# Kernel tuning notes

Hardware: AMD Instinct MI355X
Metric: run time of the kernel (lower is better)

## Reference

```python
import jax, jax.numpy as jnp
import numpy as np

EMBED = 512
HEADS = 64
DK = EMBED // HEADS  # == n_wires_attn == 8
NW_FFN = 8
FFN = 2048
EPS = 1e-5


def _layernorm(x, g, b):
    mu = jnp.mean(x, axis=-1, keepdims=True)
    var = jnp.var(x, axis=-1, keepdims=True)
    return (x - mu) * jax.lax.rsqrt(var + EPS) * g + b


def setup_inputs() -> dict:
    key = jax.random.key(0)
    ks = jax.random.split(key, 12)
    d = {
        "x": jax.random.normal(ks[0], (4, 1024, EMBED), dtype=jnp.float32),
        # attention quantum RX params (one per wire, shared across heads/tokens)
        "phi": jax.random.normal(ks[1], (DK,), dtype=jnp.float32) * 0.1,
        # combine_heads linear
        "Wc": jax.random.normal(ks[2], (EMBED, EMBED), dtype=jnp.float32) / np.sqrt(EMBED),
        "bc": jnp.zeros((EMBED,), dtype=jnp.float32),
        # FFN quantum RY params
        "theta": jax.random.normal(ks[3], (NW_FFN,), dtype=jnp.float32) * 0.1,
        "W1": jax.random.normal(ks[4], (NW_FFN, FFN), dtype=jnp.float32) / np.sqrt(NW_FFN),
        "b1": jnp.zeros((FFN,), dtype=jnp.float32),
        "W2": jax.random.normal(ks[5], (FFN, EMBED), dtype=jnp.float32) / np.sqrt(FFN),
        "b2": jnp.zeros((EMBED,), dtype=jnp.float32),
        "g1": jnp.ones((EMBED,), dtype=jnp.float32),
        "be1": jnp.zeros((EMBED,), dtype=jnp.float32),
        "g2": jnp.ones((EMBED,), dtype=jnp.float32),
        "be2": jnp.zeros((EMBED,), dtype=jnp.float32),
    }
    return d


def reference(x, phi, Wc, bc, theta, W1, b1, W2, b2, g1, be1, g2, be2):
    B, S, E = x.shape
    # --- quantum attention projections ---
    # Per head-row of DK features: RX(x_i) encoder then trainable RX(phi_i),
    xh = x.reshape(B, S, HEADS, DK)
    qkv = jnp.cos(xh + phi)                     # [B,S,H,DK]
    qkv = jnp.transpose(qkv, (0, 2, 1, 3))      # [B,H,S,DK]
    scores = jnp.einsum('bhqd,bhkd->bhqk', qkv, qkv) / jnp.sqrt(jnp.float32(DK))
    attn = jax.nn.softmax(scores, axis=-1)
    out = jnp.einsum('bhqk,bhkd->bhqd', attn, qkv)
    out = jnp.transpose(out, (0, 2, 1, 3)).reshape(B, S, E)
    attn_out = out @ Wc.T if False else out @ Wc + bc  # combine_heads linear
    x1 = _layernorm(x + attn_out, g1, be1)
    # --- quantum FFN: RX(x_i) then trainable RY(theta_i) -> <Z> = cos(x_i)*cos(theta_i)
    qout = jnp.cos(x1[..., :NW_FFN]) * jnp.cos(theta)   # [B,S,NW_FFN]
    h = jax.nn.relu(qout @ W1 + b1)
    ffn_out = h @ W2 + b2
    return _layernorm(x1 + ffn_out, g2, be2)
```

## Files before the change

kernel.cpp:

```cpp
#include <hip/hip_runtime.h>
#include <hip/hip_bf16.h>
#include <math.h>

#define B 4
#define S 1024
#define E 512
#define H 64
#define DK 8
#define FFN 2048
#define BS (B*S)

#define CSCALE 0.7141879f

#if __has_builtin(__builtin_amdgcn_exp2f)
#define EXP2F(x) __builtin_amdgcn_exp2f(x)
#else
#define EXP2F(x) exp2f(x)
#endif

typedef __attribute__((ext_vector_type(8))) short short8;
typedef __attribute__((ext_vector_type(4))) float float4a;

union U8 { short8 v; unsigned u[4]; };
union F4 { float4a v; float f[4]; };

__device__ __forceinline__ unsigned short f2bf(float f) {
    unsigned u = __builtin_bit_cast(unsigned, f);
    u = (u + 0x7fffu + ((u >> 16) & 1u)) >> 16;
    return (unsigned short)u;
}
__device__ __forceinline__ float bf2f(unsigned short h) {
    return __builtin_bit_cast(float, (unsigned)h << 16);
}
__device__ __forceinline__ unsigned packbf(float a, float b) {
    return __builtin_amdgcn_perm(__builtin_bit_cast(unsigned, a),
                                 __builtin_bit_cast(unsigned, b), 0x07060302u);
}
__device__ __forceinline__ unsigned packbf_rn(float a, float b) {
    return ((unsigned)f2bf(a) << 16) | f2bf(b);
}
__device__ __forceinline__ int pidx(int k) {
    return (k & ~31) | (((k >> 2) & 3) << 3) | (((k >> 4) & 1) << 2) | (k & 3);
}

__global__ __launch_bounds__(512) void attn_conv_kernel(const float* __restrict__ x,
                                                        const float* __restrict__ phi,
                                                        const float* __restrict__ Wc,
                                                        const float* __restrict__ W2,
                                                        const float* __restrict__ W1,
                                                        const float* __restrict__ b1,
                                                        unsigned short* __restrict__ Afrag,
                                                        unsigned short* __restrict__ W2f,
                                                        unsigned short* __restrict__ Wcf,
                                                        unsigned short* __restrict__ W1f) {
    __shared__ unsigned short kv[(S + 16) * DK];
    __shared__ unsigned short vtp[9][S + 8];
    int bid = blockIdx.x;
    int tid = threadIdx.x;

    if (bid >= 1024) {
        int idx = (bid - 1024) * 512 + tid;
        if (idx < 131072) {
            int lane = idx & 63, c = idx >> 6;
            int ntile = c >> 6, kb32 = c & 63;
            int g = lane >> 4, col = lane & 15;
            int n = ntile * 16 + col, kb = kb32 * 32;
            short8 o;
            #pragma unroll
            for (int j = 0; j < 8; j++) {
                int k = kb + 16 * (j >> 2) + 4 * g + (j & 3);
                o[j] = (short)f2bf(W2[(size_t)k * 512 + n]);
            }
            *(short8*)&W2f[(size_t)idx * 8] = o;
        } else if (idx < 163840) {
            int i2 = idx - 131072;
            int lane = i2 & 63, c = i2 >> 6;
            int ntile = c >> 4, kb32 = c & 15;
            int g = lane >> 4, col = lane & 15;
            int n = ntile * 16 + col, kb = kb32 * 32;
            short8 o;
            #pragma unroll
            for (int j = 0; j < 8; j++)
                o[j] = (short)f2bf(Wc[(size_t)(kb + g * 8 + j) * 512 + n]);
            *(short8*)&Wcf[(size_t)i2 * 8] = o;
        } else {
            int i3 = idx - 163840;
            int lane = i3 & 63, c = i3 >> 6;
            int g = lane >> 4, col = lane & 15;
            int f = (c >> 1) * 32 + (c & 1) * 16 + col;
            short8 o = {0,0,0,0,0,0,0,0};
            if (g == 0) {
                #pragma unroll
                for (int j = 0; j < 8; j++) o[j] = (short)f2bf(W1[j * FFN + f]);
            } else if (g == 1) {
                o[0] = (short)f2bf(b1[f]);
            }
            *(short8*)&W1f[(size_t)i3 * 8] = o;
        }
        return;
    }

    int head = bid >> 2, qquad = bid & 3;
    int b = head >> 6, hh = head & 63;

    float ph[DK];
    #pragma unroll
    for (int d = 0; d < DK; d++) ph[d] = phi[d];

    const short8 z8 = {0,0,0,0,0,0,0,0};
    {
        int r2 = tid * 2;
        unsigned short vb[8][2];
        #pragma unroll
        for (int j = 0; j < 2; j++) {
            const float* xp = x + ((size_t)(b * S + r2 + j)) * E + hh * DK;
            float4 u = *(const float4*)xp;
            float4 v = *(const float4*)(xp + 4);
            float c[8] = {__cosf(u.x+ph[0]), __cosf(u.y+ph[1]), __cosf(u.z+ph[2]), __cosf(u.w+ph[3]),
                          __cosf(v.x+ph[4]), __cosf(v.y+ph[5]), __cosf(v.z+ph[6]), __cosf(v.w+ph[7])};
            U8 kr;
            kr.u[0] = packbf_rn(c[1] * CSCALE, c[0] * CSCALE);
            kr.u[1] = packbf_rn(c[3] * CSCALE, c[2] * CSCALE);
            kr.u[2] = packbf_rn(c[5] * CSCALE, c[4] * CSCALE);
            kr.u[3] = packbf_rn(c[7] * CSCALE, c[6] * CSCALE);
            *(short8*)&kv[(r2 + j) * DK] = kr.v;
            #pragma unroll
            for (int d = 0; d < 8; d++) vb[d][j] = f2bf(c[d]);
        }
        int pr = pidx(r2);
        #pragma unroll
        for (int d = 0; d < 8; d++)
            *(unsigned*)&vtp[d][pr] = (unsigned)vb[d][0] | ((unsigned)vb[d][1] << 16);
        *(unsigned*)&vtp[8][pr] = 0x3F803F80u;
    }
    if (tid < 16) *(short8*)&kv[(S + tid) * DK] = z8;
    __syncthreads();

    int w = tid >> 6, lane = tid & 63, col = lane & 15, g = lane >> 4;
    bool g0 = (g == 0);
    int q0 = qquad * 256 + w * 32;
    const float4a zc = {0.f,0.f,0.f,0.f};

    short8 aq[2];
    #pragma unroll
    for (int t = 0; t < 2; t++)
        aq[t] = g0 ? *(const short8*)&kv[(q0 + t*16 + col) * DK] : z8;

    float4a acc[2];
    acc[0] = zc; acc[1] = zc;

    int vrow = col < 8 ? col : 8;
    const unsigned short* vbase = &vtp[vrow][0];

    int off0 = g0 ? col * DK : S * DK;
    int off1 = g0 ? (16 + col) * DK : S * DK;
    int stepo = g0 ? 32 * DK : 0;

    for (int kb = 0; kb < S; kb += 32) {
        short8 bk0 = *(const short8*)&kv[off0];
        short8 bk1 = *(const short8*)&kv[off1];
        off0 += stepo; off1 += stepo;
        short8 vf = *(const short8*)(vbase + kb + g * 8);
        #pragma unroll
        for (int t = 0; t < 2; t++) {
            float4a s0 = __builtin_amdgcn_mfma_f32_16x16x32_bf16(bk0, aq[t], zc, 0,0,0);
            float4a s1 = __builtin_amdgcn_mfma_f32_16x16x32_bf16(bk1, aq[t], zc, 0,0,0);
            F4 S0, S1; S0.v = s0; S1.v = s1;
            float e00 = EXP2F(S0.f[0]);
            float e01 = EXP2F(S0.f[1]);
            float e02 = EXP2F(S0.f[2]);
            float e03 = EXP2F(S0.f[3]);
            float e10 = EXP2F(S1.f[0]);
            float e11 = EXP2F(S1.f[1]);
            float e12 = EXP2F(S1.f[2]);
            float e13 = EXP2F(S1.f[3]);
            U8 pf;
            pf.u[0] = packbf(e01, e00);
            pf.u[1] = packbf(e03, e02);
            pf.u[2] = packbf(e11, e10);
            pf.u[3] = packbf(e13, e12);
            acc[t] = __builtin_amdgcn_mfma_f32_16x16x32_bf16(vf, pf.v, acc[t], 0,0,0);
        }
    }
    int lp8 = ((hh & 3) * 16 + col) * 8;
    #pragma unroll
    for (int t = 0; t < 2; t++) {
        F4 a; a.v = acc[t];
        float denom = __shfl(a.f[0], 32 + col);
        float inv = __builtin_amdgcn_rcpf(denom);
        if (g < 2) {
            int chunk = (hh >> 2) * 256 + (b * 64 + qquad * 16 + w * 2 + t);
            uint2 o;
            o.x = packbf_rn(a.f[1] * inv, a.f[0] * inv);
            o.y = packbf_rn(a.f[3] * inv, a.f[2] * inv);
            *(uint2*)&Afrag[(size_t)chunk * 512 + lp8 + g * 4] = o;
        }
    }
}

__global__ __launch_bounds__(512) void combine_ln1(const unsigned short* __restrict__ Afrag,
                                                   const unsigned short* __restrict__ Wcf,
                                                   const float* __restrict__ bc,
                                                   const float* __restrict__ x,
                                                   const float* __restrict__ g1,
                                                   const float* __restrict__ be1,
                                                   float* __restrict__ x1out,
                                                   unsigned short* __restrict__ qoutbf,
                                                   const float* __restrict__ theta) {
    __shared__ unsigned short As[16 * 64 * 8];
    __shared__ float xout[16][516];
    int tt = blockIdx.x;
    int tid = threadIdx.x;

    for (int i = tid; i < 1024; i += 512)
        *(short8*)&As[i * 8] =
            *(const short8*)&Afrag[((size_t)((i >> 6) * 256 + tt) * 64 + (i & 63)) * 8];
    __syncthreads();

    int w = tid >> 6, lane = tid & 63, col = lane & 15, g = lane >> 4;
    const float4a zc = {0.f,0.f,0.f,0.f};
    float4a acc[4];
    #pragma unroll
    for (int nt = 0; nt < 4; nt++) acc[nt] = zc;

    for (int kb32 = 0; kb32 < 16; kb32++) {
        short8 af = *(const short8*)&As[(kb32 * 64 + lane) * 8];
        #pragma unroll
        for (int nt = 0; nt < 4; nt++) {
            short8 bf = *(const short8*)&Wcf[((size_t)((w * 4 + nt) * 16 + kb32) * 64 + lane) * 8];
            acc[nt] = __builtin_amdgcn_mfma_f32_16x16x32_bf16(af, bf, acc[nt], 0, 0, 0);
        }
    }
    #pragma unroll
    for (int nt = 0; nt < 4; nt++) {
        int n = w * 64 + nt * 16 + col;
        float bb = bc[n];
        #pragma unroll
        for (int r = 0; r < 4; r++)
            xout[g * 4 + r][n] = acc[nt][r] + bb;
    }
    __syncthreads();

    int hl = lane >> 5, l = lane & 31;
    int token = w * 2 + hl;
    int e0 = l * 16;
    size_t grow = ((size_t)tt * 16 + token) * 512;
    float v[16];
    float s = 0.f, sq = 0.f;
    #pragma unroll
    for (int u = 0; u < 4; u++) {
        float4 xv = *(const float4*)&x[grow + e0 + u * 4];
        float4 pv = *(const float4*)&xout[token][e0 + u * 4];
        float a0 = xv.x + pv.x, a1 = xv.y + pv.y, a2 = xv.z + pv.z, a3 = xv.w + pv.w;
        v[u*4] = a0; v[u*4+1] = a1; v[u*4+2] = a2; v[u*4+3] = a3;
        s += a0 + a1 + a2 + a3;
        sq += a0*a0 + a1*a1 + a2*a2 + a3*a3;
    }
    #pragma unroll
    for (int off = 1; off <= 16; off <<= 1) {
        s  += __shfl_xor(s, off);
        sq += __shfl_xor(sq, off);
    }
    float mu = s * (1.f / 512.f);
    float var = sq * (1.f / 512.f) - mu * mu;
    float rstd = rsqrtf(var + 1e-5f);
    float y[16];
    #pragma unroll
    for (int u = 0; u < 4; u++) {
        float4 gv = *(const float4*)&g1[e0 + u * 4];
        float4 bv = *(const float4*)&be1[e0 + u * 4];
        y[u*4]   = (v[u*4]   - mu) * rstd * gv.x + bv.x;
        y[u*4+1] = (v[u*4+1] - mu) * rstd * gv.y + bv.y;
        y[u*4+2] = (v[u*4+2] - mu) * rstd * gv.z + bv.z;
        y[u*4+3] = (v[u*4+3] - mu) * rstd * gv.w + bv.w;
        float4 o = make_float4(y[u*4], y[u*4+1], y[u*4+2], y[u*4+3]);
        *(float4*)&x1out[grow + e0 + u * 4] = o;
    }
    if (l == 0) {
        U8 q;
        q.u[0] = packbf_rn(__cosf(y[1]) * __cosf(theta[1]), __cosf(y[0]) * __cosf(theta[0]));
        q.u[1] = packbf_rn(__cosf(y[3]) * __cosf(theta[3]), __cosf(y[2]) * __cosf(theta[2]));
        q.u[2] = packbf_rn(__cosf(y[5]) * __cosf(theta[5]), __cosf(y[4]) * __cosf(theta[4]));
        q.u[3] = packbf_rn(__cosf(y[7]) * __cosf(theta[7]), __cosf(y[6]) * __cosf(theta[6]));
        *(short8*)&qoutbf[((size_t)tt * 16 + token) * 8] = q.v;
    }
}

__global__ __launch_bounds__(512) void ffn_mfma(const unsigned short* __restrict__ qbf,
                                                const unsigned short* __restrict__ W1fg,
                                                const unsigned short* __restrict__ W2f,
                                                const float* __restrict__ b2,
                                                unsigned short* __restrict__ Cbf) {
    __shared__ unsigned short w1x[FFN * 16];
    int tid = threadIdx.x;
    #pragma unroll
    for (int i = 0; i < 8; i++) {
        int d = tid + i * 512;
        int f = d >> 1, gg = d & 1;
        int kb32 = f >> 5, half = (f >> 4) & 1, fc = f & 15;
        int src = ((kb32 * 2 + half) * 64 + gg * 16 + fc);
        *(short8*)&w1x[f * 16 + gg * 8] = *(const short8*)&W1fg[(size_t)src * 8];
    }
    __syncthreads();

    int w = tid >> 6, lane = tid & 63, col = lane & 15, g = lane >> 4;
    int mw = blockIdx.x * 256 + w * 32;
    int ntile0 = blockIdx.y * 2;
    const short8 z8 = {0,0,0,0,0,0,0,0};
    const short8 one8 = {(short)0x3F80,0,0,0,0,0,0,0};
    const float4a zc = {0.f,0.f,0.f,0.f};

    short8 qf[2];
    #pragma unroll
    for (int t = 0; t < 2; t++)
        qf[t] = (g == 0) ? *(const short8*)&qbf[(size_t)(mw + t * 16 + col) * 8]
                         : (g == 1 ? one8 : z8);

    float4a acc[2][2];
    acc[0][0] = zc; acc[0][1] = zc; acc[1][0] = zc; acc[1][1] = zc;

    const unsigned short* w2p0 = W2f + (size_t)(ntile0 * 64) * 512 + lane * 8;
    const unsigned short* w2p1 = W2f + (size_t)((ntile0 + 1) * 64) * 512 + lane * 8;

    for (int kb32 = 0; kb32 < 64; kb32++) {
        int kb = kb32 * 32;
        short8 w1f0 = (g < 2) ? *(const short8*)&w1x[(kb + col) * 16 + g * 8] : z8;
        short8 w1f1 = (g < 2) ? *(const short8*)&w1x[(kb + 16 + col) * 16 + g * 8] : z8;
        short8 af0 = *(const short8*)(w2p0 + (size_t)kb32 * 512);
        short8 af1 = *(const short8*)(w2p1 + (size_t)kb32 * 512);
        #pragma unroll
        for (int t = 0; t < 2; t++) {
            float4a h0 = __builtin_amdgcn_mfma_f32_16x16x32_bf16(w1f0, qf[t], zc, 0,0,0);
            float4a h1 = __builtin_amdgcn_mfma_f32_16x16x32_bf16(w1f1, qf[t], zc, 0,0,0);
            F4 H0, H1; H0.v = h0; H1.v = h1;
            float e00 = fmaxf(H0.f[0], 0.f);
            float e01 = fmaxf(H0.f[1], 0.f);
            float e02 = fmaxf(H0.f[2], 0.f);
            float e03 = fmaxf(H0.f[3], 0.f);
            float e10 = fmaxf(H1.f[0], 0.f);
            float e11 = fmaxf(H1.f[1], 0.f);
            float e12 = fmaxf(H1.f[2], 0.f);
            float e13 = fmaxf(H1.f[3], 0.f);
            U8 pf;
            pf.u[0] = packbf(e01, e00);
            pf.u[1] = packbf(e03, e02);
            pf.u[2] = packbf(e11, e10);
            pf.u[3] = packbf(e13, e12);
            acc[t][0] = __builtin_amdgcn_mfma_f32_16x16x32_bf16(af0, pf.v, acc[t][0], 0,0,0);
            acc[t][1] = __builtin_amdgcn_mfma_f32_16x16x32_bf16(af1, pf.v, acc[t][1], 0,0,0);
        }
    }
    int n0 = ntile0 * 16;
    #pragma unroll
    for (int nt = 0; nt < 2; nt++) {
        float4 bb = *(const float4*)&b2[n0 + nt * 16 + 4 * g];
        #pragma unroll
        for (int t = 0; t < 2; t++) {
            F4 a; a.v = acc[t][nt];
            uint2 o;
            o.x = packbf_rn(a.f[1] + bb.y, a.f[0] + bb.x);
            o.y = packbf_rn(a.f[3] + bb.w, a.f[2] + bb.z);
            *(uint2*)&Cbf[(size_t)(mw + t * 16 + col) * 512 + n0 + nt * 16 + 4 * g] = o;
        }
    }
}

__global__ __launch_bounds__(256) void ln_kernel(const float* a,
                                                 const unsigned short* __restrict__ r,
                                                 const float* __restrict__ g,
                                                 const float* __restrict__ be,
                                                 float* out) {
    int t = blockIdx.x, tid = threadIdx.x;
    size_t base = (size_t)t * E;
    int e0 = tid * 2;
    float2 av = *(const float2*)&a[base + e0];
    unsigned rv = *(const unsigned*)&r[base + e0];
    float v0 = av.x + bf2f((unsigned short)(rv & 0xffff));
    float v1 = av.y + bf2f((unsigned short)(rv >> 16));
    float s  = v0 + v1;
    float sq = v0 * v0 + v1 * v1;
    #pragma unroll
    for (int off = 32; off > 0; off >>= 1) {
        s  += __shfl_down(s, off);
        sq += __shfl_down(sq, off);
    }
    __shared__ float ls[4], lq[4];
    int wave = tid >> 6, lane = tid & 63;
    if (lane == 0) { ls[wave] = s; lq[wave] = sq; }
    __syncthreads();
    if (tid == 0) {
        float SS = ls[0] + ls[1] + ls[2] + ls[3];
        float QQ = lq[0] + lq[1] + lq[2] + lq[3];
        float mu = SS * (1.f / E);
        float var = QQ * (1.f / E) - mu * mu;
        ls[0] = mu;
        lq[0] = rsqrtf(var + 1e-5f);
    }
    __syncthreads();
    float mu = ls[0], rstd = lq[0];
    float2 gv = *(const float2*)&g[e0];
    float2 bv = *(const float2*)&be[e0];
    float y0 = (v0 - mu) * rstd * gv.x + bv.x;
    float y1 = (v1 - mu) * rstd * gv.y + bv.y;
    *(float2*)&out[base + e0] = make_float2(y0, y1);
}

extern "C" void kernel_launch(void* const* d_in, const int* in_sizes, int n_in,
                              void* d_out, int out_size, void* d_ws, size_t ws_size,
                              hipStream_t stream) {
    const float* x     = (const float*)d_in[0];
    const float* phi   = (const float*)d_in[1];
    const float* Wc    = (const float*)d_in[2];
    const float* bc    = (const float*)d_in[3];
    const float* theta = (const float*)d_in[4];
    const float* W1    = (const float*)d_in[5];
    const float* b1    = (const float*)d_in[6];
    const float* W2    = (const float*)d_in[7];
    const float* b2    = (const float*)d_in[8];
    const float* g1    = (const float*)d_in[9];
    const float* be1   = (const float*)d_in[10];
    const float* g2    = (const float*)d_in[11];
    const float* be2   = (const float*)d_in[12];
    float* out = (float*)d_out;

    float* ws = (float*)d_ws;
    unsigned short* Afrag  = (unsigned short*)ws;
    unsigned short* W2f    = (unsigned short*)(ws + 1048576);
    unsigned short* Wcf    = (unsigned short*)(ws + 1572864);
    unsigned short* W1f    = (unsigned short*)(ws + 1703936);
    unsigned short* qoutbf = (unsigned short*)(ws + 1736704);

    attn_conv_kernel<<<1360, 512, 0, stream>>>(x, phi, Wc, W2, W1, b1,
                                               Afrag, W2f, Wcf, W1f);
    combine_ln1<<<256, 512, 0, stream>>>(Afrag, Wcf, bc, x, g1, be1,
                                         out, qoutbf, theta);
    ffn_mfma<<<dim3(16, 16), 512, 0, stream>>>(qoutbf, W1f, W2f, b2, Afrag);
    ln_kernel<<<BS, 256, 0, stream>>>(out, Afrag, g2, be2, out);
}
```

Before: 161.4 us.

## Stage Wc through LDS with async double-buffering and shrink FFN tiles

The weight-conversion blocks now run first in the attention kernel, and the W1 fragment layout is compacted so ffn_mfma can load it straight into LDS with global_load_lds. combine_ln1 now streams Wc fragments into a double-buffered LDS ring with async global-to-LDS copies and explicit waitcnt and barriers, where before it read them from global memory inside the MFMA loop. ffn_mfma is retiled to one 16-row by 16-column tile per wave on a 32x32 grid, giving four times as many blocks but less reuse of each W2 fragment. This trades more recomputation of the W1 hidden layer and more W2 traffic for higher occupancy and parallelism.

```diff
diff --git a/kernel.cpp b/kernel.cpp
--- a/kernel.cpp
+++ b/kernel.cpp
@@ -41,6 +41,12 @@
 }
 __device__ __forceinline__ int pidx(int k) {
     return (k & ~31) | (((k >> 2) & 3) << 3) | (((k >> 4) & 1) << 2) | (k & 3);
+}
+
+__device__ __forceinline__ void glds16(const void* g, void* l) {
+    __builtin_amdgcn_global_load_lds(
+        (const __attribute__((address_space(1))) void*)g,
+        (__attribute__((address_space(3))) void*)l, 16, 0, 0);
 }
 
 __global__ __launch_bounds__(512) void attn_conv_kernel(const float* __restrict__ x,
@@ -57,9 +63,10 @@
     __shared__ unsigned short vtp[9][S + 8];
     int bid = blockIdx.x;
     int tid = threadIdx.x;
-
-    if (bid >= 1024) {
-        int idx = (bid - 1024) * 512 + tid;
+    const short8 z8 = {0,0,0,0,0,0,0,0};
+
+    if (bid < 336) {
+        int idx = bid * 512 + tid;
         if (idx < 131072) {
             int lane = idx & 63, c = idx >> 6;
             int ntile = c >> 6, kb32 = c & 63;
@@ -85,29 +92,29 @@
             *(short8*)&Wcf[(size_t)i2 * 8] = o;
         } else {
             int i3 = idx - 163840;
-            int lane = i3 & 63, c = i3 >> 6;
-            int g = lane >> 4, col = lane & 15;
-            int f = (c >> 1) * 32 + (c & 1) * 16 + col;
-            short8 o = {0,0,0,0,0,0,0,0};
-            if (g == 0) {
-                #pragma unroll
-                for (int j = 0; j < 8; j++) o[j] = (short)f2bf(W1[j * FFN + f]);
-            } else if (g == 1) {
-                o[0] = (short)f2bf(b1[f]);
+            if (i3 < 4096) {
+                int f = i3 >> 1, gg = i3 & 1;
+                short8 o = z8;
+                if (gg == 0) {
+                    #pragma unroll
+                    for (int j = 0; j < 8; j++) o[j] = (short)f2bf(W1[j * FFN + f]);
+                } else {
+                    o[0] = (short)f2bf(b1[f]);
+                }
+                *(short8*)&W1f[(size_t)i3 * 8] = o;
             }
-            *(short8*)&W1f[(size_t)i3 * 8] = o;
         }
         return;
     }
 
-    int head = bid >> 2, qquad = bid & 3;
+    int abid = bid - 336;
+    int head = abid >> 2, qquad = abid & 3;
     int b = head >> 6, hh = head & 63;
 
     float ph[DK];
     #pragma unroll
     for (int d = 0; d < DK; d++) ph[d] = phi[d];
 
-    const short8 z8 = {0,0,0,0,0,0,0,0};
     {
         int r2 = tid * 2;
         unsigned short vb[8][2];
@@ -208,27 +215,61 @@
                                                    unsigned short* __restrict__ qoutbf,
                                                    const float* __restrict__ theta) {
     __shared__ unsigned short As[16 * 64 * 8];
+    __shared__ unsigned short Wcs[2][2048 * 8];
     __shared__ float xout[16][516];
     int tt = blockIdx.x;
     int tid = threadIdx.x;
-
-    for (int i = tid; i < 1024; i += 512)
-        *(short8*)&As[i * 8] =
-            *(const short8*)&Afrag[((size_t)((i >> 6) * 256 + tt) * 64 + (i & 63)) * 8];
-    __syncthreads();
-
-    int w = tid >> 6, lane = tid & 63, col = lane & 15, g = lane >> 4;
+    int w = tid >> 6, lane = tid & 63;
+    int wbase = (tid & ~63) * 8;
+
+    #pragma unroll
+    for (int r = 0; r < 2; r++) {
+        const unsigned short* gsrc =
+            Afrag + ((size_t)((r * 8 + w) * 256 + tt) * 64 + lane) * 8;
+        glds16(gsrc, &As[r * 4096 + wbase]);
+    }
+    #pragma unroll
+    for (int r = 0; r < 4; r++) {
+        int nt = r * 8 + w;
+        glds16(Wcf + ((size_t)(nt * 16 + 0) * 64 + lane) * 8, &Wcs[0][nt * 512]);
+    }
+    #pragma unroll
+    for (int r = 0; r < 4; r++) {
+        int nt = r * 8 + w;
+        glds16(Wcf + ((size_t)(nt * 16 + 1) * 64 + lane) * 8, &Wcs[1][nt * 512]);
+    }
+    asm volatile("s_waitcnt vmcnt(4)" ::: "memory");
+    __builtin_amdgcn_s_barrier();
+
+    int col = lane & 15, g = lane >> 4;
     const float4a zc = {0.f,0.f,0.f,0.f};
     float4a acc[4];
     #pragma unroll
     for (int nt = 0; nt < 4; nt++) acc[nt] = zc;
 
     for (int kb32 = 0; kb32 < 16; kb32++) {
+        int cur = kb32 & 1;
         short8 af = *(const short8*)&As[(kb32 * 64 + lane) * 8];
         #pragma unroll
         for (int nt = 0; nt < 4; nt++) {
-            short8 bf = *(const short8*)&Wcf[((size_t)((w * 4 + nt) * 16 + kb32) * 64 + lane) * 8];
+            short8 bf = *(const short8*)&Wcs[cur][((w * 4 + nt) * 64 + lane) * 8];
             acc[nt] = __builtin_amdgcn_mfma_f32_16x16x32_bf16(af, bf, acc[nt], 0, 0, 0);
+        }
+        if (kb32 < 15) {
+            asm volatile("s_waitcnt lgkmcnt(0)" ::: "memory");
+            __builtin_amdgcn_s_barrier();
+            if (kb32 < 14) {
+                #pragma unroll
+                for (int r = 0; r < 4; r++) {
+                    int nt = r * 8 + w;
+                    glds16(Wcf + ((size_t)(nt * 16 + kb32 + 2) * 64 + lane) * 8,
+                           &Wcs[cur][nt * 512]);
+                }
+                asm volatile("s_waitcnt vmcnt(4)" ::: "memory");
+            } else {
+                asm volatile("s_waitcnt vmcnt(0)" ::: "memory");
+            }
+            __builtin_amdgcn_s_barrier();
         }
     }
     #pragma unroll
@@ -293,76 +334,56 @@
                                                 unsigned short* __restrict__ Cbf) {
     __shared__ unsigned short w1x[FFN * 16];
     int tid = threadIdx.x;
-    #pragma unroll
-    for (int i = 0; i < 8; i++) {
-        int d = tid + i * 512;
-        int f = d >> 1, gg = d & 1;
-        int kb32 = f >> 5, half = (f >> 4) & 1, fc = f & 15;
-        int src = ((kb32 * 2 + half) * 64 + gg * 16 + fc);
-        *(short8*)&w1x[f * 16 + gg * 8] = *(const short8*)&W1fg[(size_t)src * 8];
-    }
+    int wbase = (tid & ~63) * 8;
+    #pragma unroll
+    for (int r = 0; r < 8; r++)
+        glds16(W1fg + (size_t)(r * 512 + tid) * 8, &w1x[r * 4096 + wbase]);
+    asm volatile("s_waitcnt vmcnt(0)" ::: "memory");
     __syncthreads();
 
     int w = tid >> 6, lane = tid & 63, col = lane & 15, g = lane >> 4;
-    int mw = blockIdx.x * 256 + w * 32;
-    int ntile0 = blockIdx.y * 2;
+    int mw = blockIdx.x * 128 + w * 16;
+    int ntile = blockIdx.y;
     const short8 z8 = {0,0,0,0,0,0,0,0};
     const short8 one8 = {(short)0x3F80,0,0,0,0,0,0,0};
     const float4a zc = {0.f,0.f,0.f,0.f};
 
-    short8 qf[2];
-    #pragma unroll
-    for (int t = 0; t < 2; t++)
-        qf[t] = (g == 0) ? *(const short8*)&qbf[(size_t)(mw + t * 16 + col) * 8]
+    short8 qf = (g == 0) ? *(const short8*)&qbf[(size_t)(mw + col) * 8]
                          : (g == 1 ? one8 : z8);
-
-    float4a acc[2][2];
-    acc[0][0] = zc; acc[0][1] = zc; acc[1][0] = zc; acc[1][1] = zc;
-
-    const unsigned short* w2p0 = W2f + (size_t)(ntile0 * 64) * 512 + lane * 8;
-    const unsigned short* w2p1 = W2f + (size_t)((ntile0 + 1) * 64) * 512 + lane * 8;
-
+    float4a acc = zc;
+    const unsigned short* w2p = W2f + (size_t)(ntile * 64) * 512 + lane * 8;
+
+    #pragma unroll 2
     for (int kb32 = 0; kb32 < 64; kb32++) {
         int kb = kb32 * 32;
         short8 w1f0 = (g < 2) ? *(const short8*)&w1x[(kb + col) * 16 + g * 8] : z8;
         short8 w1f1 = (g < 2) ? *(const short8*)&w1x[(kb + 16 + col) * 16 + g * 8] : z8;
-        short8 af0 = *(const short8*)(w2p0 + (size_t)kb32 * 512);
-        short8 af1 = *(const short8*)(w2p1 + (size_t)kb32 * 512);
-        #pragma unroll
-        for (int t = 0; t < 2; t++) {
-            float4a h0 = __builtin_amdgcn_mfma_f32_16x16x32_bf16(w1f0, qf[t], zc, 0,0,0);
-            float4a h1 = __builtin_amdgcn_mfma_f32_16x16x32_bf16(w1f1, qf[t], zc, 0,0,0);
-            F4 H0, H1; H0.v = h0; H1.v = h1;
-            float e00 = fmaxf(H0.f[0], 0.f);
-            float e01 = fmaxf(H0.f[1], 0.f);
-            float e02 = fmaxf(H0.f[2], 0.f);
-            float e03 = fmaxf(H0.f[3], 0.f);
-            float e10 = fmaxf(H1.f[0], 0.f);
-            float e11 = fmaxf(H1.f[1], 0.f);
-            float e12 = fmaxf(H1.f[2], 0.f);
-            float e13 = fmaxf(H1.f[3], 0.f);
-            U8 pf;
-            pf.u[0] = packbf(e01, e00);
-            pf.u[1] = packbf(e03, e02);
-            pf.u[2] = packbf(e11, e10);
-            pf.u[3] = packbf(e13, e12);
-            acc[t][0] = __builtin_amdgcn_mfma_f32_16x16x32_bf16(af0, pf.v, acc[t][0], 0,0,0);
-            acc[t][1] = __builtin_amdgcn_mfma_f32_16x16x32_bf16(af1, pf.v, acc[t][1], 0,0,0);
-        }
-    }
-    int n0 = ntile0 * 16;
-    #pragma unroll
-    for (int nt = 0; nt < 2; nt++) {
-        float4 bb = *(const float4*)&b2[n0 + nt * 16 + 4 * g];
-        #pragma unroll
-        for (int t = 0; t < 2; t++) {
-            F4 a; a.v = acc[t][nt];
-            uint2 o;
-            o.x = packbf_rn(a.f[1] + bb.y, a.f[0] + bb.x);
-            o.y = packbf_rn(a.f[3] + bb.w, a.f[2] + bb.z);
-            *(uint2*)&Cbf[(size_t)(mw + t * 16 + col) * 512 + n0 + nt * 16 + 4 * g] = o;
-        }
-    }
+        short8 af = *(const short8*)(w2p + (size_t)kb32 * 512);
+        float4a h0 = __builtin_amdgcn_mfma_f32_16x16x32_bf16(w1f0, qf, zc, 0,0,0);
+        float4a h1 = __builtin_amdgcn_mfma_f32_16x16x32_bf16(w1f1, qf, zc, 0,0,0);
+        F4 H0, H1; H0.v = h0; H1.v = h1;
+        float e00 = fmaxf(H0.f[0], 0.f);
+        float e01 = fmaxf(H0.f[1], 0.f);
+        float e02 = fmaxf(H0.f[2], 0.f);
+        float e03 = fmaxf(H0.f[3], 0.f);
+        float e10 = fmaxf(H1.f[0], 0.f);
+        float e11 = fmaxf(H1.f[1], 0.f);
+        float e12 = fmaxf(H1.f[2], 0.f);
+        float e13 = fmaxf(H1.f[3], 0.f);
+        U8 pf;
+        pf.u[0] = packbf(e01, e00);
+        pf.u[1] = packbf(e03, e02);
+        pf.u[2] = packbf(e11, e10);
+        pf.u[3] = packbf(e13, e12);
+        acc = __builtin_amdgcn_mfma_f32_16x16x32_bf16(af, pf.v, acc, 0,0,0);
+    }
+    int n0 = ntile * 16;
+    F4 a; a.v = acc;
+    float4 bb = *(const float4*)&b2[n0 + 4 * g];
+    uint2 o;
+    o.x = packbf_rn(a.f[1] + bb.y, a.f[0] + bb.x);
+    o.y = packbf_rn(a.f[3] + bb.w, a.f[2] + bb.z);
+    *(uint2*)&Cbf[(size_t)(mw + col) * 512 + n0 + 4 * g] = o;
 }
 
 __global__ __launch_bounds__(256) void ln_kernel(const float* a,
@@ -434,6 +455,6 @@
                                                Afrag, W2f, Wcf, W1f);
     combine_ln1<<<256, 512, 0, stream>>>(Afrag, Wcf, bc, x, g1, be1,
                                          out, qoutbf, theta);
-    ffn_mfma<<<dim3(16, 16), 512, 0, stream>>>(qoutbf, W1f, W2f, b2, Afrag);
+    ffn_mfma<<<dim3(32, 32), 512, 0, stream>>>(qoutbf, W1f, W2f, b2, Afrag);
     ln_kernel<<<BS, 256, 0, stream>>>(out, Afrag, g2, be2, out);
 }
```

New measurement: 185.4 us. +14.9%, slower.
